# Optimization experiments

Hardware: AMD Instinct MI355X
Metric: run time of the kernel (lower is better)

Reference implementation:

```python
import jax, jax.numpy as jnp
import numpy as np
import math

B, S, E, H, FF = 8, 1024, 1024, 16, 4096
HD = E // H
N_DOM = 1024          # boolean-domain size used in the custom scale
LN_EPS = 1e-5


def _layernorm(x, g, b, eps=LN_EPS):
    mu = jnp.mean(x, axis=-1, keepdims=True)
    var = jnp.var(x, axis=-1, keepdims=True)
    return (x - mu) * jax.lax.rsqrt(var + eps) * g + b


def setup_inputs() -> dict:
    key = jax.random.key(0)
    ks = jax.random.split(key, 8)
    s_e = 1.0 / math.sqrt(E)
    s_f = 1.0 / math.sqrt(FF)
    return {
        "x": jax.random.normal(ks[0], (B, S, E), jnp.float32),
        "in_proj_w": jax.random.normal(ks[1], (3 * E, E), jnp.float32) * s_e,
        "out_proj_w": jax.random.normal(ks[2], (E, E), jnp.float32) * s_e,
        "ln1_g": jnp.ones((E,), jnp.float32),
        "ln1_b": jnp.zeros((E,), jnp.float32),
        "ln2_g": jnp.ones((E,), jnp.float32),
        "ln2_b": jnp.zeros((E,), jnp.float32),
        "w1": jax.random.normal(ks[3], (FF, E), jnp.float32) * s_e,
        "b1": jax.random.normal(ks[4], (FF,), jnp.float32) * 0.01,
        "w2": jax.random.normal(ks[5], (E, FF), jnp.float32) * s_f,
        "b2": jax.random.normal(ks[6], (E,), jnp.float32) * 0.01,
    }


def reference(x, in_proj_w, out_proj_w, ln1_g, ln1_b, ln2_g, ln2_b, w1, b1, w2, b2):
    # --- custom multi-head attention (bias=False, dropout=0) ---
    qkv = jnp.einsum("bse,fe->bsf", x, in_proj_w)              # [B,S,3E]
    q, k, v = jnp.split(qkv, 3, axis=-1)
    q = q.reshape(B, S, H, HD)
    k = k.reshape(B, S, H, HD)
    v = v.reshape(B, S, H, HD)
    # nonstandard scale: sqrt(1/head_dim) * 2 * log(N)
    scale = math.sqrt(1.0 / HD) * 2.0 * math.log(N_DOM)
    scores = jnp.einsum("bqhd,bkhd->bhqk", q * scale, k)       # [B,H,S,S]
    attn = jax.nn.softmax(scores, axis=-1)
    ctx = jnp.einsum("bhqk,bkhd->bqhd", attn, v).reshape(B, S, E)
    attn_out = jnp.einsum("bse,fe->bsf", ctx, out_proj_w)      # [B,S,E]
    # --- residual + norm + FFN + residual + norm ---
    h = _layernorm(x + attn_out, ln1_g, ln1_b)
    ff = jnp.einsum("bsf,ef->bse", jax.nn.relu(jnp.einsum("bse,fe->bsf", h, w1) + b1), w2) + b2
    return _layernorm(h + ff, ln2_g, ln2_b)
```

## Files before the change

kernel.cpp:

```cpp
#include <hip/hip_runtime.h>
#include <cstdint>
#include <cmath>


typedef _Float16 f16;
typedef _Float16 f16x8 __attribute__((ext_vector_type(8)));
typedef _Float16 f16x4 __attribute__((ext_vector_type(4)));
typedef __bf16   bf16;
typedef __bf16   bf16x8 __attribute__((ext_vector_type(8)));
typedef __bf16   bf16x4 __attribute__((ext_vector_type(4)));
typedef __bf16   bf16x2 __attribute__((ext_vector_type(2)));
typedef float    f32x4  __attribute__((ext_vector_type(4)));
typedef float    f32x16 __attribute__((ext_vector_type(16)));
typedef unsigned int uint2v __attribute__((ext_vector_type(2)));
typedef unsigned int u32x4v __attribute__((ext_vector_type(4)));

#define B_SZ  8
#define S_SZ  1024
#define E_SZ  1024
#define H_SZ  16
#define HD_SZ 64
#define FF_SZ 4096
#define MTOK  (B_SZ * S_SZ)

__device__ __forceinline__ void async_ld16(const void* g, void* l) {
  __builtin_amdgcn_global_load_lds(
      (const __attribute__((address_space(1))) void*)(uintptr_t)g,
      (__attribute__((address_space(3))) void*)(uint32_t)(uintptr_t)l,
      16, 0, 0);
}

template <int N>
__device__ __forceinline__ void wait_vm() {
  if constexpr (N == 0)      asm volatile("s_waitcnt vmcnt(0)" ::: "memory");
  else if constexpr (N == 3) asm volatile("s_waitcnt vmcnt(3)" ::: "memory");
  else if constexpr (N == 4) asm volatile("s_waitcnt vmcnt(4)" ::: "memory");
  else static_assert(N == 0 || N == 3 || N == 4, "unsupported vmcnt");
  __builtin_amdgcn_sched_barrier(0);
}

__device__ __forceinline__ void wait_lgkm0_fenced() {
  asm volatile("s_waitcnt lgkmcnt(0)" ::: "memory");
  __builtin_amdgcn_sched_barrier(0);
}

__device__ __forceinline__ void permswap(uint32_t& a, uint32_t& b) {
  uint2v r = __builtin_amdgcn_permlane32_swap(a, b, false, false);
  a = r[0];
  b = r[1];
}

__global__ void cast_all_kernel(const float* __restrict__ wqkv, const float* __restrict__ wo,
                                const float* __restrict__ w1, const float* __restrict__ w2,
                                const float* __restrict__ x,
                                f16* __restrict__ w_inb, f16* __restrict__ w_outb,
                                f16* __restrict__ w1b, f16* __restrict__ w2b,
                                f16* __restrict__ xb) {
  const int i = blockIdx.x * blockDim.x + threadIdx.x;
  const float* src;
  f16* dst;
  int off;
  if (i < 786432)       { src = wqkv; dst = w_inb;  off = i; }
  else if (i < 1048576) { src = wo;   dst = w_outb; off = i - 786432; }
  else if (i < 2097152) { src = w1;   dst = w1b;    off = i - 1048576; }
  else if (i < 3145728) { src = w2;   dst = w2b;    off = i - 2097152; }
  else                  { src = x;    dst = xb;     off = i - 3145728; }
  float4 f = ((const float4*)src)[off];
  f16x4 o = {(f16)f.x, (f16)f.y, (f16)f.z, (f16)f.w};
  ((f16x4*)dst)[off] = o;
}

template <int BN, bool OUT_F16, bool RELU>
__global__ __launch_bounds__(512, 2)
void gemm256(const f16* __restrict__ A, const f16* __restrict__ Bm,
             const float* __restrict__ bias, void* __restrict__ Cp,
             int M, int N, int K, int bf16_from_col) {
  static_assert(BN == 256 || BN == 128, "BN must be 256 or 128");
  static_assert(!(OUT_F16 && BN == 128), "f16 LDS epilogue requires BN==256");
  constexpr int NBCH  = (BN == 256) ? 2 : 1;
  constexpr int CHUNK = 4096;
  constexpr int NIF   = 2 + NBCH;
  constexpr int WN    = (BN == 256) ? 4 : 2;
  constexpr int FM    = (BN == 256) ? 8 : 4;

  __shared__ f16 lds[(8 + 4 * NBCH) * CHUNK];
  f16* Ab = lds;
  f16* Bb = lds + 8 * CHUNK;

  const int tid  = threadIdx.x;
  const int wave = tid >> 6;
  const int lane = tid & 63;
  const int quad = lane >> 4;
  const int l16  = lane & 15;

  const int wm  = wave / WN;
  const int wn  = wave % WN;
  const int ah  = (BN == 256) ? wm : (wm >> 1);
  const int amB = (BN == 256) ? 0 : (wm & 1) * 64;
  const int bh  = (BN == 256) ? (wn >> 1) : 0;
  const int bnB = (BN == 256) ? (wn & 1) * 64 : wn * 64;

  const int gx = N / BN;
  int bm, bn;
  {
    const int b   = blockIdx.x;
    const int nwg = gridDim.x;
    const int gm  = nwg / gx;
    if (((nwg & 63) == 0) && ((gx & 1) == 0) && ((gm & 3) == 0)) {
      const int xcd = b & 7;
      const int seq = b >> 3;
      const int st  = xcd + ((seq >> 3) << 3);
      const int pos = seq & 7;
      const int nstx = gx >> 1;
      bn = (st % nstx) * 2 + (pos & 1);
      bm = (st / nstx) * 4 + (pos >> 1);
    } else {
      int logical = b;
      if ((nwg & 7) == 0) logical = (logical & 7) * (nwg >> 3) + (logical >> 3);
      bn = logical % gx;
      bm = logical / gx;
    }
  }

  f32x4 acc[FM][4];
#pragma unroll
  for (int mi = 0; mi < FM; mi++)
#pragma unroll
    for (int ni = 0; ni < 4; ni++) acc[mi][ni] = (f32x4){0.f, 0.f, 0.f, 0.f};

  const int rr_s = tid >> 2;
  const int lo_s = (tid & 3) ^ ((rr_s >> 1) & 3);
  const int wofs = wave * 512;
  const f16* gAb = A  + ((size_t)bm * 256 + rr_s) * (size_t)K + lo_s * 8;
  const f16* gBb = Bm + ((size_t)bn * BN  + rr_s) * (size_t)K + lo_s * 8;

  auto stA = [&](int bb, int s, int h, int kt) {
    async_ld16(gAb + (size_t)h * 128 * K + kt * 64 + s * 32,
               Ab + ((((bb << 1) + s) << 1) + h) * CHUNK + wofs);
  };
  auto stB = [&](int bb, int s, int h, int kt) {
    async_ld16(gBb + (size_t)h * 128 * K + kt * 64 + s * 32,
               Bb + (((bb << 1) + s) * NBCH + h) * CHUNK + wofs);
  };
  auto rdFrag = [&](const f16* ch, int rr) -> f16x8 {
    return *(const f16x8*)&ch[rr * 32 + ((quad ^ ((rr >> 1) & 3)) << 3)];
  };

  const int NT = K >> 6;

#pragma unroll
  for (int s = 0; s < 2; s++) {
    stA(0, s, 0, 0);
    stA(0, s, 1, 0);
    stB(0, s, 0, 0);
    if constexpr (NBCH == 2) stB(0, s, 1, 0);
  }
  wait_vm<NIF>();
  __builtin_amdgcn_s_barrier();

  for (int t = 0; t < NT; t++) {
    const int cur = t & 1, oth = cur ^ 1;
    const bool last = (t == NT - 1);
#pragma unroll
    for (int s = 0; s < 2; s++) {
      const f16* Ach = Ab + ((((cur << 1) + s) << 1) + ah) * CHUNK;
      const f16* Bch = Bb + (((cur << 1) + s) * NBCH + bh) * CHUNK;

      f16x8 bfr[4], af[4];
#pragma unroll
      for (int ni = 0; ni < 4; ni++) bfr[ni] = rdFrag(Bch, bnB + ni * 16 + l16);
#pragma unroll
      for (int i = 0; i < 4; i++) af[i] = rdFrag(Ach, amB + i * 16 + l16);
      if (!last) {
        stA(oth, s, 0, t + 1);
        stA(oth, s, 1, t + 1);
        if constexpr (NBCH == 1) stB(oth, s, 0, t + 1);
      }
      __builtin_amdgcn_sched_barrier(0);
      __builtin_amdgcn_s_barrier();
      wait_lgkm0_fenced();
      __builtin_amdgcn_s_setprio(1);
#pragma unroll
      for (int i = 0; i < 4; i++)
#pragma unroll
        for (int ni = 0; ni < 4; ni++)
          acc[i][ni] = __builtin_amdgcn_mfma_f32_16x16x32_f16(bfr[ni], af[i], acc[i][ni], 0, 0, 0);
      __builtin_amdgcn_s_setprio(0);

      if constexpr (BN == 256) {
        __builtin_amdgcn_s_barrier();
#pragma unroll
        for (int i = 0; i < 4; i++) af[i] = rdFrag(Ach, amB + (4 + i) * 16 + l16);
        if (!last) {
          stB(oth, s, 0, t + 1);
          stB(oth, s, 1, t + 1);
        }
        __builtin_amdgcn_sched_barrier(0);
        __builtin_amdgcn_s_barrier();
        wait_lgkm0_fenced();
        __builtin_amdgcn_s_setprio(1);
#pragma unroll
        for (int i = 0; i < 4; i++)
#pragma unroll
          for (int ni = 0; ni < 4; ni++)
            acc[4 + i][ni] = __builtin_amdgcn_mfma_f32_16x16x32_f16(bfr[ni], af[i], acc[4 + i][ni], 0, 0, 0);
        __builtin_amdgcn_s_setprio(0);
      }

      if (!last) {
        wait_vm<NIF>();
        __builtin_amdgcn_s_barrier();
      } else if (s == 0) {
        wait_vm<0>();
        __builtin_amdgcn_s_barrier();
      }
    }
  }

  if constexpr (!OUT_F16) {
    const int rowG0 = bm * 256 + ((BN == 256) ? wm * 128 : wm * 64);
    const int colG0 = bn * BN + wn * 64;
    float* Cf = (float*)Cp;
#pragma unroll
    for (int ni = 0; ni < 4; ni++) {
      const int col = colG0 + ni * 16 + quad * 4;
      float4 bv = {0.f, 0.f, 0.f, 0.f};
      if (bias != nullptr) bv = *(const float4*)&bias[col];
#pragma unroll
      for (int mi = 0; mi < FM; mi++) {
        const int row = rowG0 + mi * 16 + l16;
        float v0 = acc[mi][ni][0] + bv.x;
        float v1 = acc[mi][ni][1] + bv.y;
        float v2 = acc[mi][ni][2] + bv.z;
        float v3 = acc[mi][ni][3] + bv.w;
        if (RELU) {
          v0 = fmaxf(v0, 0.f); v1 = fmaxf(v1, 0.f);
          v2 = fmaxf(v2, 0.f); v3 = fmaxf(v3, 0.f);
        }
        f32x4 o = {v0, v1, v2, v3};
        *(f32x4*)&Cf[(size_t)row * N + col] = o;
      }
    }
  } else {
    __syncthreads();
    {
      char* cb = (char*)lds;
      const int rowL0 = wm * 128;
      const int colL0 = wn * 64;
      const bool store_bf16 = (bn * BN >= bf16_from_col);
#pragma unroll
      for (int mi = 0; mi < FM; mi++) {
        const int row = rowL0 + mi * 16 + l16;
        const int sw  = row & 7;
#pragma unroll
        for (int ni = 0; ni < 4; ni++) {
          const int col = colL0 + ni * 16 + quad * 4;
          float4 bv = {0.f, 0.f, 0.f, 0.f};
          if (bias != nullptr) bv = *(const float4*)&bias[bn * BN + col];
          float v0 = acc[mi][ni][0] + bv.x;
          float v1 = acc[mi][ni][1] + bv.y;
          float v2 = acc[mi][ni][2] + bv.z;
          float v3 = acc[mi][ni][3] + bv.w;
          if (RELU) {
            v0 = fmaxf(v0, 0.f); v1 = fmaxf(v1, 0.f);
            v2 = fmaxf(v2, 0.f); v3 = fmaxf(v3, 0.f);
          }
          const int ch = (col >> 3) ^ sw;
          char* p = cb + row * 512 + (ch << 4) + ((quad & 1) << 3);
          if (store_bf16) {
            bf16x4 o = {(bf16)v0, (bf16)v1, (bf16)v2, (bf16)v3};
            *(bf16x4*)p = o;
          } else {
            f16x4 o = {(f16)v0, (f16)v1, (f16)v2, (f16)v3};
            *(f16x4*)p = o;
          }
        }
      }
    }
    __syncthreads();
    {
      const char* cb = (const char*)lds;
      const int rr0 = tid >> 5;
      const int cc  = tid & 31;
      const size_t rowBytes = (size_t)N * 2;
      char* gbase = (char*)Cp + (size_t)(bm * 256) * rowBytes
                  + (size_t)bn * BN * 2 + (size_t)cc * 16;
#pragma unroll
      for (int it = 0; it < 16; it++) {
        const int row = it * 16 + rr0;
        const int ch  = cc ^ (row & 7);
        u32x4v v = *(const u32x4v*)(cb + row * 512 + (ch << 4));
        *(u32x4v*)(gbase + (size_t)row * rowBytes) = v;
      }
    }
  }
  (void)M;
}

__global__ __launch_bounds__(256, 3)
void attn_kernel(const f16* __restrict__ qkv, f16* __restrict__ ctx,
                 float scale2, float c2) {
  __shared__ __align__(16) char pool[49664];
  bf16* Vt = (bf16*)(pool + 32768);

  const int tid  = threadIdx.x;
  const int wave = tid >> 6;
  const int lane = tid & 63;
  const int l31  = lane & 31;
  const int hi   = lane >> 5;

  const int flat = blockIdx.x;
  const int bh   = flat & 127;
  const int qt   = flat >> 7;
  const int b    = bh >> 4;
  const int h    = bh & 15;

  const int rs = 3 * E_SZ;
  const size_t tokbase = (size_t)b * S_SZ;

  const int su  = lane >> 3;
  const int soc = (lane & 7) ^ su;

  {
    const f16* gq = qkv + (tokbase + qt * 128 + wave * 8 + su) * (size_t)rs + h * HD_SZ + soc * 8;
#pragma unroll
    for (int i = 0; i < 4; i++)
      async_ld16(gq + (size_t)i * 32 * rs, pool + (i * 32 + wave * 8) * 128);
  }
  __syncthreads();

  f16x8 aq[4];
  {
    const f16* Q0 = (const f16*)pool;
    const int qrow = wave * 32 + l31;
    const f16 sc = (f16)scale2;
    const f16x8 sc8 = {sc, sc, sc, sc, sc, sc, sc, sc};
#pragma unroll
    for (int ks = 0; ks < 4; ks++) {
      f16x8 q = *(const f16x8*)&Q0[qrow * 64 + (((ks * 2 + hi) ^ (qrow & 7)) << 3)];
      aq[ks] = q * sc8;
    }
  }
  __syncthreads();

  const int vc  = (tid & 7) * 8;
  const int vk0 = (tid >> 3) * 4;

  {
    const f16* gk = qkv + (tokbase + 0 * 128 + wave * 8 + su) * (size_t)rs + E_SZ + h * HD_SZ + soc * 8;
#pragma unroll
    for (int i = 0; i < 4; i++)
      async_ld16(gk + (size_t)i * 32 * rs, pool + (i * 32 + wave * 8) * 128);
  }
  bf16x8 vr0, vr1, vr2, vr3;
  {
    const bf16* gv = (const bf16*)qkv + (tokbase + 0 * 128 + vk0) * (size_t)rs + 2 * E_SZ + h * HD_SZ + vc;
    vr0 = *(const bf16x8*)(gv);
    vr1 = *(const bf16x8*)(gv + rs);
    vr2 = *(const bf16x8*)(gv + 2 * rs);
    vr3 = *(const bf16x8*)(gv + 3 * rs);
  }

  f32x16 oacc[2];
  f32x16 Lacc;
#pragma unroll
  for (int nb = 0; nb < 2; nb++)
#pragma unroll
    for (int i = 0; i < 16; i++) oacc[nb][i] = 0.f;
#pragma unroll
  for (int i = 0; i < 16; i++) Lacc[i] = 0.f;

  const bf16 one = (bf16)1.0f;
  const bf16x8 onesb = {one, one, one, one, one, one, one, one};
  const float negc2 = -c2;

  for (int t = 0; t < S_SZ / 128; t++) {
    __syncthreads();
    {
#pragma unroll
      for (int e = 0; e < 8; e++) {
        bf16x4 pk = {vr0[e], vr1[e], vr2[e], vr3[e]};
        *(bf16x4*)&Vt[(vc + e) * 132 + vk0] = pk;
      }
    }
    __syncthreads();

    if (t < S_SZ / 128 - 1) {
      const f16* gk = qkv + (tokbase + (t + 1) * 128 + wave * 8 + su) * (size_t)rs + E_SZ + h * HD_SZ + soc * 8;
#pragma unroll
      for (int i = 0; i < 4; i++)
        async_ld16(gk + (size_t)i * 32 * rs, pool + ((t + 1) & 1) * 16384 + (i * 32 + wave * 8) * 128);
      const bf16* gv = (const bf16*)qkv + (tokbase + (t + 1) * 128 + vk0) * (size_t)rs + 2 * E_SZ + h * HD_SZ + vc;
      vr0 = *(const bf16x8*)(gv);
      vr1 = *(const bf16x8*)(gv + rs);
      vr2 = *(const bf16x8*)(gv + 2 * rs);
      vr3 = *(const bf16x8*)(gv + 3 * rs);
    }

    const f16* Kcur = (const f16*)(pool + (t & 1) * 16384);

#pragma unroll
    for (int nt = 0; nt < 4; nt++) {
      f32x16 sacc;
#pragma unroll
      for (int i = 0; i < 16; i++) sacc[i] = negc2;

      const int krow = nt * 32 + l31;
      __builtin_amdgcn_s_setprio(1);
#pragma unroll
      for (int ks = 0; ks < 4; ks++) {
        f16x8 kf = *(const f16x8*)&Kcur[krow * 64 + (((ks * 2 + hi) ^ (krow & 7)) << 3)];
        sacc = __builtin_amdgcn_mfma_f32_32x32x16_f16(kf, aq[ks], sacc, 0, 0, 0);
      }
      __builtin_amdgcn_s_setprio(0);

      uint32_t w[8];
#pragma unroll
      for (int j = 0; j < 8; j++) {
        float p0 = exp2f(sacc[2 * j]);
        float p1 = exp2f(sacc[2 * j + 1]);
        bf16x2 pk2 = {(bf16)p0, (bf16)p1};
        w[j] = __builtin_bit_cast(uint32_t, pk2);
      }
      permswap(w[0], w[2]);
      permswap(w[1], w[3]);
      permswap(w[4], w[6]);
      permswap(w[5], w[7]);
      u32x4v pe = {w[0], w[1], w[2], w[3]};
      u32x4v po = {w[4], w[5], w[6], w[7]};
      bf16x8 pa[2] = {__builtin_bit_cast(bf16x8, pe), __builtin_bit_cast(bf16x8, po)};

      __builtin_amdgcn_s_setprio(1);
      Lacc = __builtin_amdgcn_mfma_f32_32x32x16_bf16(pa[0], onesb, Lacc, 0, 0, 0);
      Lacc = __builtin_amdgcn_mfma_f32_32x32x16_bf16(pa[1], onesb, Lacc, 0, 0, 0);
#pragma unroll
      for (int nb = 0; nb < 2; nb++) {
        const int d = nb * 32 + l31;
#pragma unroll
        for (int kst = 0; kst < 2; kst++) {
          const int key = (nt * 2 + kst) * 16 + hi * 8;
          bf16x4 blo = *(const bf16x4*)&Vt[d * 132 + key];
          bf16x4 bhi = *(const bf16x4*)&Vt[d * 132 + key + 4];
          bf16x8 bv = __builtin_shufflevector(blo, bhi, 0, 1, 2, 3, 4, 5, 6, 7);
          oacc[nb] = __builtin_amdgcn_mfma_f32_32x32x16_bf16(pa[kst], bv, oacc[nb], 0, 0, 0);
        }
      }
      __builtin_amdgcn_s_setprio(0);
    }
  }

#pragma unroll
  for (int r = 0; r < 16; r++) {
    const float invr = 1.f / Lacc[r];
    const int qrow = (r & 3) + 8 * (r >> 2) + 4 * hi;
    const size_t row = tokbase + (size_t)qt * 128 + wave * 32 + qrow;
#pragma unroll
    for (int nb = 0; nb < 2; nb++)
      ctx[row * (size_t)E_SZ + h * HD_SZ + nb * 32 + l31] = (f16)(oacc[nb][r] * invr);
  }
}

__global__ void ln_kernel(const float* __restrict__ a, const float* __restrict__ res,
                          const float* __restrict__ g, const float* __restrict__ bta,
                          float* __restrict__ out32, f16* __restrict__ out16) {
  const int row  = blockIdx.x;
  const int tid  = threadIdx.x;
  const int wave = tid >> 6;
  const int lane = tid & 63;
  const size_t base = (size_t)row * 1024;
  const int c = tid * 4;

  float4 va = *(const float4*)&a[base + c];
  float4 vr = *(const float4*)&res[base + c];
  float v0 = va.x + vr.x, v1 = va.y + vr.y, v2 = va.z + vr.z, v3 = va.w + vr.w;

  __shared__ float r1[4], r2[4];
  float s = v0 + v1 + v2 + v3;
#pragma unroll
  for (int off = 32; off; off >>= 1) s += __shfl_xor(s, off, 64);
  if (lane == 0) r1[wave] = s;
  __syncthreads();
  const float mu = (r1[0] + r1[1] + r1[2] + r1[3]) * (1.f / 1024.f);

  float d0 = v0 - mu, d1 = v1 - mu, d2 = v2 - mu, d3 = v3 - mu;
  float ss = d0 * d0 + d1 * d1 + d2 * d2 + d3 * d3;
#pragma unroll
  for (int off = 32; off; off >>= 1) ss += __shfl_xor(ss, off, 64);
  if (lane == 0) r2[wave] = ss;
  __syncthreads();
  const float var = (r2[0] + r2[1] + r2[2] + r2[3]) * (1.f / 1024.f);
  const float rsq = rsqrtf(var + 1e-5f);

  float4 gg = *(const float4*)&g[c];
  float4 bb = *(const float4*)&bta[c];
  float o0 = d0 * rsq * gg.x + bb.x;
  float o1 = d1 * rsq * gg.y + bb.y;
  float o2 = d2 * rsq * gg.z + bb.z;
  float o3 = d3 * rsq * gg.w + bb.w;
  float4 o = {o0, o1, o2, o3};
  *(float4*)&out32[base + c] = o;
  if (out16 != nullptr) {
    f16x4 ob = {(f16)o0, (f16)o1, (f16)o2, (f16)o3};
    *(f16x4*)&out16[base + c] = ob;
  }
}

extern "C" void kernel_launch(void* const* d_in, const int* in_sizes, int n_in,
                              void* d_out, int out_size, void* d_ws, size_t ws_size,
                              hipStream_t stream) {
  const float* x    = (const float*)d_in[0];
  const float* wqkv = (const float*)d_in[1];
  const float* wo   = (const float*)d_in[2];
  const float* ln1g = (const float*)d_in[3];
  const float* ln1b = (const float*)d_in[4];
  const float* ln2g = (const float*)d_in[5];
  const float* ln2b = (const float*)d_in[6];
  const float* w1   = (const float*)d_in[7];
  const float* b1   = (const float*)d_in[8];
  const float* w2   = (const float*)d_in[9];
  const float* b2   = (const float*)d_in[10];
  float* out = (float*)d_out;

  char* ws = (char*)d_ws;
  f16* w_inb  = (f16*)(ws + 0);
  f16* w_outb = (f16*)(ws + 6291456);
  f16* w1b    = (f16*)(ws + 8388608);
  f16* w2b    = (f16*)(ws + 16777216);
  f16* xb     = (f16*)(ws + 25165824);
  f16* qkv    = (f16*)(ws + 41943040);
  f16* ctx    = (f16*)(ws + 92274688);
  f16* ff1    = (f16*)(ws + 41943040);
  float* tmp  = (float*)(ws + 109051904);
  float* hbuf = (float*)(ws + 142606336);
  f16* hb     = xb;

  const int NOBF = 1 << 30;

  cast_all_kernel<<<20480, 256, 0, stream>>>(wqkv, wo, w1, w2, x,
                                             w_inb, w_outb, w1b, w2b, xb);

  gemm256<256, true, false><<<(3 * E_SZ / 256) * (MTOK / 256), 512, 0, stream>>>(
      xb, w_inb, nullptr, qkv, MTOK, 3 * E_SZ, E_SZ, 2048);

  attn_kernel<<<1024, 256, 0, stream>>>(qkv, ctx, 2.5f, 60.0f);

  gemm256<128, false, false><<<(E_SZ / 128) * (MTOK / 256), 512, 0, stream>>>(
      ctx, w_outb, nullptr, tmp, MTOK, E_SZ, E_SZ, NOBF);

  ln_kernel<<<MTOK, 256, 0, stream>>>(tmp, x, ln1g, ln1b, hbuf, hb);

  gemm256<256, true, true><<<(FF_SZ / 256) * (MTOK / 256), 512, 0, stream>>>(
      hb, w1b, b1, ff1, MTOK, FF_SZ, E_SZ, NOBF);

  gemm256<128, false, false><<<(E_SZ / 128) * (MTOK / 256), 512, 0, stream>>>(
      ff1, w2b, b2, tmp, MTOK, E_SZ, FF_SZ, NOBF);

  ln_kernel<<<MTOK, 256, 0, stream>>>(tmp, hbuf, ln2g, ln2b, out, nullptr);

  (void)in_sizes; (void)n_in; (void)out_size; (void)ws_size;
}
```

Measured before the change: 489.3 us.

## Single-buffer K via registers and compute softmax row sums with scalar adds

Replaces the double-buffered async K tile in LDS with register prefetch plus a single LDS buffer, cutting shared memory so the attention kernel can target four blocks per CU instead of three. The softmax denominator is now accumulated as a per-lane scalar sum of the fp32 exponentials and combined with a cross-half shuffle, instead of two extra MFMAs against a ones vector per tile. This frees the accumulator registers and MFMA issue slots. The cost is weaker load/compute overlap, because K must be written to LDS behind a barrier each iteration, and possible register pressure at the higher occupancy target.

```diff
diff --git a/kernel.cpp b/kernel.cpp
--- a/kernel.cpp
+++ b/kernel.cpp
@@ -297,11 +297,12 @@
   (void)M;
 }
 
-__global__ __launch_bounds__(256, 3)
+__global__ __launch_bounds__(256, 4)
 void attn_kernel(const f16* __restrict__ qkv, f16* __restrict__ ctx,
                  float scale2, float c2) {
-  __shared__ __align__(16) char pool[49664];
-  bf16* Vt = (bf16*)(pool + 32768);
+  __shared__ __align__(16) char pool[33280];
+  f16*  Ks = (f16*)pool;
+  bf16* Vt = (bf16*)(pool + 16384);
 
   const int tid  = threadIdx.x;
   const int wave = tid >> 6;
@@ -331,52 +332,49 @@
 
   f16x8 aq[4];
   {
-    const f16* Q0 = (const f16*)pool;
     const int qrow = wave * 32 + l31;
     const f16 sc = (f16)scale2;
     const f16x8 sc8 = {sc, sc, sc, sc, sc, sc, sc, sc};
 #pragma unroll
     for (int ks = 0; ks < 4; ks++) {
-      f16x8 q = *(const f16x8*)&Q0[qrow * 64 + (((ks * 2 + hi) ^ (qrow & 7)) << 3)];
+      f16x8 q = *(const f16x8*)&Ks[qrow * 64 + (((ks * 2 + hi) ^ (qrow & 7)) << 3)];
       aq[ks] = q * sc8;
     }
   }
-  __syncthreads();
-
+
+  f16x8  kreg[4];
+  bf16x8 vr0, vr1, vr2, vr3;
   const int vc  = (tid & 7) * 8;
   const int vk0 = (tid >> 3) * 4;
-
   {
-    const f16* gk = qkv + (tokbase + 0 * 128 + wave * 8 + su) * (size_t)rs + E_SZ + h * HD_SZ + soc * 8;
-#pragma unroll
-    for (int i = 0; i < 4; i++)
-      async_ld16(gk + (size_t)i * 32 * rs, pool + (i * 32 + wave * 8) * 128);
-  }
-  bf16x8 vr0, vr1, vr2, vr3;
-  {
-    const bf16* gv = (const bf16*)qkv + (tokbase + 0 * 128 + vk0) * (size_t)rs + 2 * E_SZ + h * HD_SZ + vc;
+    const f16* gk = qkv + (tokbase + wave * 8 + su) * (size_t)rs + E_SZ + h * HD_SZ + soc * 8;
+#pragma unroll
+    for (int i = 0; i < 4; i++) kreg[i] = *(const f16x8*)(gk + (size_t)i * 32 * rs);
+    const bf16* gv = (const bf16*)qkv + (tokbase + vk0) * (size_t)rs + 2 * E_SZ + h * HD_SZ + vc;
     vr0 = *(const bf16x8*)(gv);
     vr1 = *(const bf16x8*)(gv + rs);
     vr2 = *(const bf16x8*)(gv + 2 * rs);
     vr3 = *(const bf16x8*)(gv + 3 * rs);
   }
 
+  float Lp = 0.f;
   f32x16 oacc[2];
-  f32x16 Lacc;
 #pragma unroll
   for (int nb = 0; nb < 2; nb++)
 #pragma unroll
     for (int i = 0; i < 16; i++) oacc[nb][i] = 0.f;
-#pragma unroll
-  for (int i = 0; i < 16; i++) Lacc[i] = 0.f;
-
-  const bf16 one = (bf16)1.0f;
-  const bf16x8 onesb = {one, one, one, one, one, one, one, one};
+
   const float negc2 = -c2;
 
   for (int t = 0; t < S_SZ / 128; t++) {
     __syncthreads();
     {
+      const int kwr = (wave * 8 + su) * 64 + (lane & 7) * 8;
+#pragma unroll
+      for (int i = 0; i < 4; i++)
+        *(f16x8*)&Ks[kwr + i * 32 * 64] = kreg[i];
+    }
+    {
 #pragma unroll
       for (int e = 0; e < 8; e++) {
         bf16x4 pk = {vr0[e], vr1[e], vr2[e], vr3[e]};
@@ -388,8 +386,7 @@
     if (t < S_SZ / 128 - 1) {
       const f16* gk = qkv + (tokbase + (t + 1) * 128 + wave * 8 + su) * (size_t)rs + E_SZ + h * HD_SZ + soc * 8;
 #pragma unroll
-      for (int i = 0; i < 4; i++)
-        async_ld16(gk + (size_t)i * 32 * rs, pool + ((t + 1) & 1) * 16384 + (i * 32 + wave * 8) * 128);
+      for (int i = 0; i < 4; i++) kreg[i] = *(const f16x8*)(gk + (size_t)i * 32 * rs);
       const bf16* gv = (const bf16*)qkv + (tokbase + (t + 1) * 128 + vk0) * (size_t)rs + 2 * E_SZ + h * HD_SZ + vc;
       vr0 = *(const bf16x8*)(gv);
       vr1 = *(const bf16x8*)(gv + rs);
@@ -397,8 +394,6 @@
       vr3 = *(const bf16x8*)(gv + 3 * rs);
     }
 
-    const f16* Kcur = (const f16*)(pool + (t & 1) * 16384);
-
 #pragma unroll
     for (int nt = 0; nt < 4; nt++) {
       f32x16 sacc;
@@ -409,7 +404,7 @@
       __builtin_amdgcn_s_setprio(1);
 #pragma unroll
       for (int ks = 0; ks < 4; ks++) {
-        f16x8 kf = *(const f16x8*)&Kcur[krow * 64 + (((ks * 2 + hi) ^ (krow & 7)) << 3)];
+        f16x8 kf = *(const f16x8*)&Ks[krow * 64 + (((ks * 2 + hi) ^ (krow & 7)) << 3)];
         sacc = __builtin_amdgcn_mfma_f32_32x32x16_f16(kf, aq[ks], sacc, 0, 0, 0);
       }
       __builtin_amdgcn_s_setprio(0);
@@ -419,6 +414,7 @@
       for (int j = 0; j < 8; j++) {
         float p0 = exp2f(sacc[2 * j]);
         float p1 = exp2f(sacc[2 * j + 1]);
+        Lp += p0 + p1;
         bf16x2 pk2 = {(bf16)p0, (bf16)p1};
         w[j] = __builtin_bit_cast(uint32_t, pk2);
       }
@@ -431,8 +427,6 @@
       bf16x8 pa[2] = {__builtin_bit_cast(bf16x8, pe), __builtin_bit_cast(bf16x8, po)};
 
       __builtin_amdgcn_s_setprio(1);
-      Lacc = __builtin_amdgcn_mfma_f32_32x32x16_bf16(pa[0], onesb, Lacc, 0, 0, 0);
-      Lacc = __builtin_amdgcn_mfma_f32_32x32x16_bf16(pa[1], onesb, Lacc, 0, 0, 0);
 #pragma unroll
       for (int nb = 0; nb < 2; nb++) {
         const int d = nb * 32 + l31;
@@ -449,10 +443,12 @@
     }
   }
 
+  float Lfull = Lp + __shfl_xor(Lp, 32, 64);
+  const float inv = 1.f / Lfull;
 #pragma unroll
   for (int r = 0; r < 16; r++) {
-    const float invr = 1.f / Lacc[r];
     const int qrow = (r & 3) + 8 * (r >> 2) + 4 * hi;
+    const float invr = __shfl(inv, qrow, 32);
     const size_t row = tokbase + (size_t)qt * 128 + wave * 32 + qrow;
 #pragma unroll
     for (int nb = 0; nb < 2; nb++)
```

Result: no change. 484.2 us (-1.1%).
